# Performance work log

Hardware: AMD Instinct MI355X
Metric: run time of the kernel (lower is better)

## Reference

```python
import jax, jax.numpy as jnp
import numpy as np

B = 16       # number of point clouds
N_PER = 2048 # points per cloud
K = 16       # knn neighbors (loop=True -> self included as nearest)
NUM_CLASSES = 10


def _linear_params(key, fan_in, fan_out):
    # torch.nn.Linear default init: U(-1/sqrt(fan_in), 1/sqrt(fan_in))
    kw, kb = jax.random.split(key)
    s = 1.0 / np.sqrt(fan_in)
    W = jax.random.uniform(kw, (fan_in, fan_out), jnp.float32, -s, s)
    b = jax.random.uniform(kb, (fan_out,), jnp.float32, -s, s)
    return W, b


def setup_inputs() -> dict:
    key = jax.random.key(0)
    ks = jax.random.split(key, 7)
    pos = jax.random.normal(ks[0], (B * N_PER, 3), jnp.float32)
    batch = jnp.repeat(jnp.arange(B, dtype=jnp.int64), N_PER)  # sorted graph ids
    W1a, b1a = _linear_params(ks[1], 3 + 3, 32)   # conv1 mlp layer 1 (h=pos -> 3+3)
    W1b, b1b = _linear_params(ks[2], 32, 32)      # conv1 mlp layer 2
    W2a, b2a = _linear_params(ks[3], 32 + 3, 32)  # conv2 mlp layer 1
    W2b, b2b = _linear_params(ks[4], 32, 32)      # conv2 mlp layer 2
    Wc, bc = _linear_params(ks[5], 32, NUM_CLASSES)
    return dict(pos=pos, batch=batch,
                W1a=W1a, b1a=b1a, W1b=W1b, b1b=b1b,
                W2a=W2a, b2a=b2a, W2b=W2b, b2b=b2b,
                Wc=Wc, bc=bc)


def _knn_idx(p):
    # p: [n,3] -> [n,K] indices of K nearest points (self included, dist 0)
    d2 = jnp.sum((p[:, None, :] - p[None, :, :]) ** 2, axis=-1)  # [n,n]
    _, idx = jax.lax.top_k(-d2, K)
    return idx


def _pointnet_layer(h, p, idx, Wa, ba, Wb, bb):
    # single graph: h [n,C], p [n,3], idx [n,K]
    h_j = h[idx]                           # gather neighbor features [n,K,C]
    spatial = p[idx] - p[:, None, :]       # pos_j - pos_i [n,K,3]
    x = jnp.concatenate([h_j, spatial], axis=-1)
    x = jax.nn.relu(x @ Wa + ba) @ Wb + bb # per-edge MLP
    return jnp.max(x, axis=1)              # max aggregation over neighbors


def reference(pos, batch, W1a, b1a, W1b, b1b, W2a, b2a, W2b, b2b, Wc, bc):
    # batch is sorted with equal-sized graphs -> reshape to [B, n, 3]
    p = pos.reshape(B, N_PER, 3)
    idx = jax.vmap(_knn_idx)(p)  # [B, n, K] dynamic knn graph
    layer = jax.vmap(_pointnet_layer, in_axes=(0, 0, 0, None, None, None, None))
    h = jax.nn.relu(layer(p, p, idx, W1a, b1a, W1b, b1b))   # [B, n, 32]
    h = jax.nn.relu(layer(h, p, idx, W2a, b2a, W2b, b2b))   # [B, n, 32]
    g = jnp.max(h, axis=1)                                   # global_max_pool [B, 32]
    return g @ Wc + bc                                       # [B, num_classes]
```

## Files before the change

kernel.cpp:

```cpp
#include <hip/hip_runtime.h>
#include <hip/hip_bf16.h>
#include <cstdint>

#define NCLOUDS 16
#define N_PER   2048
#define KNN_K   16
#define CAP     48

typedef unsigned long long u64;
#define INFF __builtin_inff()

template <int J>
__device__ __forceinline__ int ixor(int x) {
    if constexpr (J == 1)
        return __builtin_amdgcn_update_dpp(0, x, 0xB1, 0xF, 0xF, true);
    else if constexpr (J == 2)
        return __builtin_amdgcn_update_dpp(0, x, 0x4E, 0xF, 0xF, true);
    else if constexpr (J <= 16)
        return __builtin_amdgcn_ds_swizzle(x, (J << 10) | 0x1F);
    else
        return __shfl_xor(x, 32);
}
template <int J> __device__ __forceinline__ float fxor(float x) {
    return __int_as_float(ixor<J>(__float_as_int(x)));
}
template <int J> __device__ __forceinline__ u64 uxor(u64 x) {
    const int lo = ixor<J>((int)(x & 0xffffffffULL));
    const int hi = ixor<J>((int)(x >> 32));
    return ((u64)(unsigned)hi << 32) | (unsigned)lo;
}

__device__ __forceinline__ float dpp_max16(float x) {
    x = fmaxf(x, __int_as_float(__builtin_amdgcn_update_dpp(0, __float_as_int(x), 0xB1, 0xF, 0xF, true)));
    x = fmaxf(x, __int_as_float(__builtin_amdgcn_update_dpp(0, __float_as_int(x), 0x4E, 0xF, 0xF, true)));
    x = fmaxf(x, __int_as_float(__builtin_amdgcn_update_dpp(0, __float_as_int(x), 0x141, 0xF, 0xF, true)));
    x = fmaxf(x, __int_as_float(__builtin_amdgcn_update_dpp(0, __float_as_int(x), 0x140, 0xF, 0xF, true)));
    return x;
}

__global__ __launch_bounds__(512) void knn_kernel(const float* __restrict__ pos,
                                                  int* __restrict__ knn_out,
                                                  const float* __restrict__ W1a,
                                                  const float* __restrict__ b1a,
                                                  float* __restrict__ w1,
                                                  float* __restrict__ v1)
{
    __shared__ float qshare[3][32];
    __shared__ float smA[4][2][8][16];
    __shared__ u64   buf[4][8][CAP];
    __shared__ int   cnt[4][8];

    const int cloud = blockIdx.x >> 6;
    const int qblk  = blockIdx.x & 63;
    const int tid   = threadIdx.x;
    const int wave  = tid >> 6;
    const int lane  = tid & 63;
    const int H     = wave & 1;
    const int pr    = wave >> 1;

    const int b0 = cloud * N_PER;

    if (tid < 32) {
        const float* qp = pos + (size_t)(b0 + qblk * 32 + tid) * 3;
        qshare[0][tid] = qp[0];
        qshare[1][tid] = qp[1];
        qshare[2][tid] = qp[2];
        ((int*)cnt)[tid] = 0;
    }

    float cx[16], cy[16], cz[16], sc[16];
#pragma unroll
    for (int jj = 0; jj < 16; ++jj) {
        const int c = H * 1024 + jj * 64 + lane;
        const float* p = pos + (size_t)(b0 + c) * 3;
        cx[jj] = p[0]; cy[jj] = p[1]; cz[jj] = p[2];
        sc[jj] = fmaf(cz[jj], cz[jj], fmaf(cy[jj], cy[jj], cx[jj] * cx[jj]));
    }
    __syncthreads();

#pragma unroll 1
    for (int t = 0; t < 4; ++t) {
        const int qg0 = pr * 8 + 2 * t, qg1 = qg0 + 1;
        const float Q0x = qshare[0][qg0], Q0y = qshare[1][qg0], Q0z = qshare[2][qg0];
        const float Q1x = qshare[0][qg1], Q1y = qshare[1][qg1], Q1z = qshare[2][qg1];
        const float A0x = -2.0f * Q0x, A0y = -2.0f * Q0y, A0z = -2.0f * Q0z;
        const float A1x = -2.0f * Q1x, A1y = -2.0f * Q1y, A1z = -2.0f * Q1z;
        float v0 = INFF, v1r = INFF;
#pragma unroll
        for (int jj = 0; jj < 16; ++jj) {
            float e0 = fmaf(cx[jj], A0x, sc[jj]);
            float e1 = fmaf(cx[jj], A1x, sc[jj]);
            e0 = fmaf(cy[jj], A0y, e0);  e1 = fmaf(cy[jj], A1y, e1);
            e0 = fmaf(cz[jj], A0z, e0);  e1 = fmaf(cz[jj], A1z, e1);
            v0 = fminf(v0, e0);          v1r = fminf(v1r, e1);
        }
#define FS(K, J) { const float o0 = fxor<J>(v0), o1 = fxor<J>(v1r);             \
                   const bool km = (((lane & J) == 0) == ((lane & K) == 0));    \
                   v0 = km ? fminf(v0, o0) : fmaxf(v0, o0);                     \
                   v1r = km ? fminf(v1r, o1) : fmaxf(v1r, o1); }
        FS(2,1)
        FS(4,2) FS(4,1)
        FS(8,4) FS(8,2) FS(8,1)
        FS(16,8) FS(16,4) FS(16,2) FS(16,1)
        FS(32,16) FS(32,8) FS(32,4) FS(32,2) FS(32,1)
        FS(64,32) FS(64,16) FS(64,8) FS(64,4) FS(64,2) FS(64,1)
#undef FS
        if (lane < 16) {
            smA[pr][H][2 * t][lane]     = v0;
            smA[pr][H][2 * t + 1][lane] = v1r;
        }
    }
    __syncthreads();

#pragma unroll 1
    for (int t = 0; t < 4; ++t) {
        const int q0 = 2 * t, q1 = q0 + 1;
        float a0 = -INFF, a1 = -INFF, b0v = -INFF, b1v = -INFF;
        if (lane > 0 && lane <= 16) {
            a0 = smA[pr][0][q0][lane - 1];
            a1 = smA[pr][0][q1][lane - 1];
        }
        if (lane < 16) {
            b0v = smA[pr][1][q0][15 - lane];
            b1v = smA[pr][1][q1][15 - lane];
        }
        float m0 = (lane <= 16) ? fmaxf(a0, b0v) : INFF;
        float m1 = (lane <= 16) ? fmaxf(a1, b1v) : INFF;
        m0 = fminf(m0, fxor<1>(m0));   m1 = fminf(m1, fxor<1>(m1));
        m0 = fminf(m0, fxor<2>(m0));   m1 = fminf(m1, fxor<2>(m1));
        m0 = fminf(m0, fxor<4>(m0));   m1 = fminf(m1, fxor<4>(m1));
        m0 = fminf(m0, fxor<8>(m0));   m1 = fminf(m1, fxor<8>(m1));
        m0 = fminf(m0, fxor<16>(m0));  m1 = fminf(m1, fxor<16>(m1));
        m0 = fminf(m0, fxor<32>(m0));  m1 = fminf(m1, fxor<32>(m1));

        const int qg0 = pr * 8 + q0, qg1 = pr * 8 + q1;
        const float Q0x = qshare[0][qg0], Q0y = qshare[1][qg0], Q0z = qshare[2][qg0];
        const float Q1x = qshare[0][qg1], Q1y = qshare[1][qg1], Q1z = qshare[2][qg1];
        const float qq0 = fmaf(Q0z, Q0z, fmaf(Q0y, Q0y, Q0x * Q0x));
        const float qq1 = fmaf(Q1z, Q1z, fmaf(Q1y, Q1y, Q1x * Q1x));
        const float T0 = (m0 + qq0) * (1.0f + 1e-5f) + 1e-4f;
        const float T1 = (m1 + qq1) * (1.0f + 1e-5f) + 1e-4f;

#pragma unroll
        for (int jj = 0; jj < 16; ++jj) {
            const int c = H * 1024 + jj * 64 + lane;
            const float dx0 = __fsub_rn(Q0x, cx[jj]);
            const float dy0 = __fsub_rn(Q0y, cy[jj]);
            const float dz0 = __fsub_rn(Q0z, cz[jj]);
            const float d20 = __fadd_rn(__fadd_rn(__fmul_rn(dx0, dx0), __fmul_rn(dy0, dy0)),
                                        __fmul_rn(dz0, dz0));
            if (d20 <= T0) {
                const int slot = atomicAdd(&cnt[pr][q0], 1);
                if (slot < CAP)
                    buf[pr][q0][slot] = ((u64)__float_as_uint(d20) << 32) | (unsigned)c;
            }
            const float dx1 = __fsub_rn(Q1x, cx[jj]);
            const float dy1 = __fsub_rn(Q1y, cy[jj]);
            const float dz1 = __fsub_rn(Q1z, cz[jj]);
            const float d21 = __fadd_rn(__fadd_rn(__fmul_rn(dx1, dx1), __fmul_rn(dy1, dy1)),
                                        __fmul_rn(dz1, dz1));
            if (d21 <= T1) {
                const int slot = atomicAdd(&cnt[pr][q1], 1);
                if (slot < CAP)
                    buf[pr][q1][slot] = ((u64)__float_as_uint(d21) << 32) | (unsigned)c;
            }
        }
    }
    __syncthreads();

#pragma unroll 1
    for (int s = 0; s < 2; ++s) {
        const int q0 = H * 4 + 2 * s, q1 = q0 + 1;
        const int n0 = min(cnt[pr][q0], CAP);
        const int n1 = min(cnt[pr][q1], CAP);
        u64 k0 = (lane < n0) ? buf[pr][q0][lane] : ~0ULL;
        u64 k1 = (lane < n1) ? buf[pr][q1][lane] : ~0ULL;
#define US(K, J) { const u64 o0 = uxor<J>(k0), o1 = uxor<J>(k1);                \
                   const bool km = (((lane & J) == 0) == ((lane & K) == 0));    \
                   const u64 l0 = k0 < o0 ? k0 : o0, h0 = k0 < o0 ? o0 : k0;    \
                   k0 = km ? l0 : h0;                                           \
                   const u64 l1 = k1 < o1 ? k1 : o1, h1 = k1 < o1 ? o1 : k1;    \
                   k1 = km ? l1 : h1; }
        US(2,1)
        US(4,2) US(4,1)
        US(8,4) US(8,2) US(8,1)
        US(16,8) US(16,4) US(16,2) US(16,1)
        US(32,16) US(32,8) US(32,4) US(32,2) US(32,1)
        US(64,32) US(64,16) US(64,8) US(64,4) US(64,2) US(64,1)
#undef US
        if (lane < KNN_K) {
            knn_out[((size_t)b0 + qblk * 32 + pr * 8 + q0) * KNN_K + lane] =
                b0 + (int)(unsigned)(k0 & 0xffffffffu);
            knn_out[((size_t)b0 + qblk * 32 + pr * 8 + q1) * KNN_K + lane] =
                b0 + (int)(unsigned)(k1 & 0xffffffffu);
        }
    }

    {
        const int pt = tid >> 4;
        const int kk = tid & 15;
        const int gp = b0 + qblk * 32 + pt;
        const float p0 = pos[3 * (size_t)gp + 0];
        const float p1 = pos[3 * (size_t)gp + 1];
        const float p2 = pos[3 * (size_t)gp + 2];
        float vA = 0.f, vB = 0.f;
        float wA = b1a[kk], wB = b1a[16 + kk];
#pragma unroll
        for (int d = 0; d < 3; ++d) {
            const float pd = d == 0 ? p0 : (d == 1 ? p1 : p2);
            wA = fmaf(pd, W1a[d * 32 + kk],        wA);
            wB = fmaf(pd, W1a[d * 32 + 16 + kk],   wB);
            vA = fmaf(pd, W1a[(3 + d) * 32 + kk],      vA);
            vB = fmaf(pd, W1a[(3 + d) * 32 + 16 + kk], vB);
        }
        w1[(size_t)gp * 32 + kk]      = wA + vA;
        w1[(size_t)gp * 32 + 16 + kk] = wB + vB;
        v1[(size_t)gp * 32 + kk]      = vA;
        v1[(size_t)gp * 32 + 16 + kk] = vB;
    }
}

template <bool FUSE_PRE2>
__global__ __launch_bounds__(256) void layer_kernel(
    const int*   __restrict__ knn,
    const float* __restrict__ Wb, const float* __restrict__ bb,
    const float* __restrict__ w,  const float* __restrict__ v,
    const float* __restrict__ pos,
    const float* __restrict__ Wna, const float* __restrict__ bna,
    float* __restrict__ outA, float* __restrict__ outB)
{
    __shared__ float h1s[16][32];

    const int gth = blockIdx.x * 256 + threadIdx.x;
    const int p = gth >> 4;
    const int k = gth & 15;
    const int j = knn[gth];

    const float4* w4 = (const float4*)w;
    const float4* v4 = (const float4*)v;

    float hid[32];
#pragma unroll
    for (int i = 0; i < 8; ++i) {
        const float4 a = w4[(size_t)j * 8 + i];
        const float4 b = v4[(size_t)p * 8 + i];
        hid[4 * i + 0] = fmaxf(a.x - b.x, 0.0f);
        hid[4 * i + 1] = fmaxf(a.y - b.y, 0.0f);
        hid[4 * i + 2] = fmaxf(a.z - b.z, 0.0f);
        hid[4 * i + 3] = fmaxf(a.w - b.w, 0.0f);
    }

    float o[32];
#pragma unroll
    for (int c2 = 0; c2 < 32; ++c2) o[c2] = bb[c2];
#pragma unroll
    for (int c = 0; c < 32; ++c) {
        const float hc = hid[c];
        const float* row = Wb + c * 32;
#pragma unroll
        for (int c2 = 0; c2 < 32; ++c2) o[c2] = fmaf(hc, row[c2], o[c2]);
    }

    float out0 = 0.0f, out1 = 0.0f;
#pragma unroll
    for (int c2 = 0; c2 < 32; ++c2) {
        const float s = dpp_max16(o[c2]);
        if ((c2 & 15) == k) { if (c2 < 16) out0 = s; else out1 = s; }
    }
    out0 = fmaxf(out0, 0.0f);
    out1 = fmaxf(out1, 0.0f);

    if constexpr (!FUSE_PRE2) {
        outA[(size_t)p * 32 + k]      = out0;
        outA[(size_t)p * 32 + 16 + k] = out1;
    } else {
        const int pl = threadIdx.x >> 4;
        h1s[pl][k]      = out0;
        h1s[pl][16 + k] = out1;
        __syncthreads();
        float accA = bna[k], accB = bna[16 + k];
#pragma unroll
        for (int c = 0; c < 32; ++c) {
            const float hc = h1s[pl][c];
            accA = fmaf(hc, Wna[c * 32 + k],      accA);
            accB = fmaf(hc, Wna[c * 32 + 16 + k], accB);
        }
        float vA = 0.f, vB = 0.f;
#pragma unroll
        for (int d = 0; d < 3; ++d) {
            const float pd = pos[3 * (size_t)p + d];
            vA = fmaf(pd, Wna[(32 + d) * 32 + k],      vA);
            vB = fmaf(pd, Wna[(32 + d) * 32 + 16 + k], vB);
        }
        outA[(size_t)p * 32 + k]      = accA + vA;
        outA[(size_t)p * 32 + 16 + k] = accB + vB;
        outB[(size_t)p * 32 + k]      = vA;
        outB[(size_t)p * 32 + 16 + k] = vB;
    }
}

__global__ __launch_bounds__(256) void pool_kernel(
    const float* __restrict__ h2, const float* __restrict__ Wc,
    const float* __restrict__ bc, float* __restrict__ out)
{
    __shared__ float red[8][32];
    __shared__ float sg[32];
    const int cloud = blockIdx.x;
    const int t = threadIdx.x;
    const int c = t & 31, row = t >> 5;
    float m = 0.0f;
    for (int p = row; p < N_PER; p += 8)
        m = fmaxf(m, h2[((size_t)cloud * N_PER + p) * 32 + c]);
    red[row][c] = m;
    __syncthreads();
    if (t < 32) {
        float gv = red[0][t];
#pragma unroll
        for (int r = 1; r < 8; ++r) gv = fmaxf(gv, red[r][t]);
        sg[t] = gv;
    }
    __syncthreads();
    if (t < 10) {
        float s = bc[t];
#pragma unroll
        for (int c0 = 0; c0 < 32; ++c0) s = fmaf(sg[c0], Wc[c0 * 10 + t], s);
        out[cloud * 10 + t] = s;
    }
}

extern "C" void kernel_launch(void* const* d_in, const int* in_sizes, int n_in,
                              void* d_out, int out_size, void* d_ws, size_t ws_size,
                              hipStream_t stream)
{
    const float* pos = (const float*)d_in[0];
    const float* W1a = (const float*)d_in[2];
    const float* b1a = (const float*)d_in[3];
    const float* W1b = (const float*)d_in[4];
    const float* b1b = (const float*)d_in[5];
    const float* W2a = (const float*)d_in[6];
    const float* b2a = (const float*)d_in[7];
    const float* W2b = (const float*)d_in[8];
    const float* b2b = (const float*)d_in[9];
    const float* Wc  = (const float*)d_in[10];
    const float* bc  = (const float*)d_in[11];

    int*   knn = (int*)d_ws;
    float* w1  = (float*)((char*)d_ws + (size_t)(2  << 20));
    float* v1  = (float*)((char*)d_ws + (size_t)(6  << 20));
    float* w2  = (float*)((char*)d_ws + (size_t)(10 << 20));
    float* v2  = (float*)((char*)d_ws + (size_t)(14 << 20));
    float* h2  = (float*)((char*)d_ws + (size_t)(18 << 20));
    float* out = (float*)d_out;

    const int npts = NCLOUDS * N_PER;

    knn_kernel<<<dim3(NCLOUDS * 64), dim3(512), 0, stream>>>(
        pos, knn, W1a, b1a, w1, v1);
    layer_kernel<true><<<dim3(npts * KNN_K / 256), dim3(256), 0, stream>>>(
        knn, W1b, b1b, w1, v1, pos, W2a, b2a, w2, v2);
    layer_kernel<false><<<dim3(npts * KNN_K / 256), dim3(256), 0, stream>>>(
        knn, W2b, b2b, w2, v2, pos, W2a, b2a, h2, nullptr);
    pool_kernel<<<dim3(NCLOUDS), dim3(256), 0, stream>>>(h2, Wc, bc, out);
}
```

Measured before the change: 151.1 us.

## Fuse global max-pool and classifier into layer-2 kernel; stage gathers in LDS

The separate pool kernel is removed. The second layer kernel now reduces its 16 points per block, does an atomicMax into a global buffer that the knn kernel zeroes, and the last block, found through an atomic counter, computes the classifier. Neighbor feature gathers are also staged into padded shared memory with cooperative float4 loads before the per-edge MLP. This saves one launch and the h2 write and read, at the cost of atomics, more LDS use (about 38KB per block, which may limit occupancy) and extra syncs.

```diff
diff --git a/kernel.cpp b/kernel.cpp
--- a/kernel.cpp
+++ b/kernel.cpp
@@ -43,7 +43,9 @@
                                                   const float* __restrict__ W1a,
                                                   const float* __restrict__ b1a,
                                                   float* __restrict__ w1,
-                                                  float* __restrict__ v1)
+                                                  float* __restrict__ v1,
+                                                  float* __restrict__ gbuf,
+                                                  int* __restrict__ counter)
 {
     __shared__ float qshare[3][32];
     __shared__ float smA[4][2][8][16];
@@ -59,6 +61,11 @@
     const int pr    = wave >> 1;
 
     const int b0 = cloud * N_PER;
+
+    if (blockIdx.x == 0) {
+        if (tid < NCLOUDS * 32) gbuf[tid] = 0.0f;
+        if (tid == 0) *counter = 0;
+    }
 
     if (tid < 32) {
         const float* qp = pos + (size_t)(b0 + qblk * 32 + tid) * 3;
@@ -220,30 +227,52 @@
     }
 }
 
-template <bool FUSE_PRE2>
+template <int MODE>
 __global__ __launch_bounds__(256) void layer_kernel(
     const int*   __restrict__ knn,
     const float* __restrict__ Wb, const float* __restrict__ bb,
     const float* __restrict__ w,  const float* __restrict__ v,
     const float* __restrict__ pos,
     const float* __restrict__ Wna, const float* __restrict__ bna,
-    float* __restrict__ outA, float* __restrict__ outB)
+    float* __restrict__ outA, float* __restrict__ outB,
+    const float* __restrict__ Wc, const float* __restrict__ bc,
+    float* __restrict__ gbuf, int* __restrict__ counter,
+    float* __restrict__ out)
 {
-    __shared__ float h1s[16][32];
-
-    const int gth = blockIdx.x * 256 + threadIdx.x;
-    const int p = gth >> 4;
-    const int k = gth & 15;
-    const int j = knn[gth];
-
-    const float4* w4 = (const float4*)w;
-    const float4* v4 = (const float4*)v;
+    __shared__ float wst[256 * 36];
+    __shared__ float vst[16 * 36];
+    __shared__ int   jl[256];
+    __shared__ int   lastFlag;
+
+    const int tid = threadIdx.x;
+    const int gth = blockIdx.x * 256 + tid;
+    const int P0  = blockIdx.x * 16;
+
+    jl[tid] = knn[gth];
+    __syncthreads();
+
+#pragma unroll
+    for (int s = 0; s < 8; ++s) {
+        const int r = s * 32 + (tid >> 3);
+        const int i = tid & 7;
+        const float4 t4 = *(const float4*)(w + (size_t)jl[r] * 32 + i * 4);
+        *(float4*)&wst[r * 36 + i * 4] = t4;
+    }
+    if (tid < 128) {
+        const int r = tid >> 3, i = tid & 7;
+        const float4 t4 = *(const float4*)(v + (size_t)(P0 + r) * 32 + i * 4);
+        *(float4*)&vst[r * 36 + i * 4] = t4;
+    }
+    __syncthreads();
+
+    const int k  = tid & 15;
+    const int pl = tid >> 4;
 
     float hid[32];
 #pragma unroll
     for (int i = 0; i < 8; ++i) {
-        const float4 a = w4[(size_t)j * 8 + i];
-        const float4 b = v4[(size_t)p * 8 + i];
+        const float4 a = *(const float4*)&wst[tid * 36 + i * 4];
+        const float4 b = *(const float4*)&vst[pl  * 36 + i * 4];
         hid[4 * i + 0] = fmaxf(a.x - b.x, 0.0f);
         hid[4 * i + 1] = fmaxf(a.y - b.y, 0.0f);
         hid[4 * i + 2] = fmaxf(a.z - b.z, 0.0f);
@@ -270,18 +299,18 @@
     out0 = fmaxf(out0, 0.0f);
     out1 = fmaxf(out1, 0.0f);
 
-    if constexpr (!FUSE_PRE2) {
-        outA[(size_t)p * 32 + k]      = out0;
-        outA[(size_t)p * 32 + 16 + k] = out1;
-    } else {
-        const int pl = threadIdx.x >> 4;
-        h1s[pl][k]      = out0;
-        h1s[pl][16 + k] = out1;
-        __syncthreads();
+    __syncthreads();
+    float* hs = wst;
+    hs[pl * 32 + k]      = out0;
+    hs[pl * 32 + 16 + k] = out1;
+    __syncthreads();
+
+    if constexpr (MODE == 1) {
+        const int p = gth >> 4;
         float accA = bna[k], accB = bna[16 + k];
 #pragma unroll
         for (int c = 0; c < 32; ++c) {
-            const float hc = h1s[pl][c];
+            const float hc = hs[pl * 32 + c];
             accA = fmaf(hc, Wna[c * 32 + k],      accA);
             accB = fmaf(hc, Wna[c * 32 + 16 + k], accB);
         }
@@ -296,35 +325,34 @@
         outA[(size_t)p * 32 + 16 + k] = accB + vB;
         outB[(size_t)p * 32 + k]      = vA;
         outB[(size_t)p * 32 + 16 + k] = vB;
-    }
-}
-
-__global__ __launch_bounds__(256) void pool_kernel(
-    const float* __restrict__ h2, const float* __restrict__ Wc,
-    const float* __restrict__ bc, float* __restrict__ out)
-{
-    __shared__ float red[8][32];
-    __shared__ float sg[32];
-    const int cloud = blockIdx.x;
-    const int t = threadIdx.x;
-    const int c = t & 31, row = t >> 5;
-    float m = 0.0f;
-    for (int p = row; p < N_PER; p += 8)
-        m = fmaxf(m, h2[((size_t)cloud * N_PER + p) * 32 + c]);
-    red[row][c] = m;
-    __syncthreads();
-    if (t < 32) {
-        float gv = red[0][t];
-#pragma unroll
-        for (int r = 1; r < 8; ++r) gv = fmaxf(gv, red[r][t]);
-        sg[t] = gv;
-    }
-    __syncthreads();
-    if (t < 10) {
-        float s = bc[t];
-#pragma unroll
-        for (int c0 = 0; c0 < 32; ++c0) s = fmaf(sg[c0], Wc[c0 * 10 + t], s);
-        out[cloud * 10 + t] = s;
+    } else {
+        if (tid < 32) {
+            float m = hs[tid];
+#pragma unroll
+            for (int p2 = 1; p2 < 16; ++p2) m = fmaxf(m, hs[p2 * 32 + tid]);
+            const int cloud = P0 >> 11;
+            atomicMax((int*)&gbuf[cloud * 32 + tid], __float_as_int(m));
+        }
+        __syncthreads();
+        if (tid == 0) {
+            __threadfence();
+            lastFlag = (atomicAdd(counter, 1) == (int)gridDim.x - 1);
+        }
+        __syncthreads();
+        if (lastFlag) {
+            float* gl = wst;
+            for (int t = tid; t < NCLOUDS * 32; t += 256)
+                gl[t] = __int_as_float(atomicMax((int*)&gbuf[t], 0));
+            __syncthreads();
+            if (tid < NCLOUDS * 10) {
+                const int cl = tid / 10, cls = tid - cl * 10;
+                float s2 = bc[cls];
+#pragma unroll
+                for (int c = 0; c < 32; ++c)
+                    s2 = fmaf(gl[cl * 32 + c], Wc[c * 10 + cls], s2);
+                out[tid] = s2;
+            }
+        }
     }
 }
 
@@ -344,21 +372,23 @@
     const float* Wc  = (const float*)d_in[10];
     const float* bc  = (const float*)d_in[11];
 
-    int*   knn = (int*)d_ws;
-    float* w1  = (float*)((char*)d_ws + (size_t)(2  << 20));
-    float* v1  = (float*)((char*)d_ws + (size_t)(6  << 20));
-    float* w2  = (float*)((char*)d_ws + (size_t)(10 << 20));
-    float* v2  = (float*)((char*)d_ws + (size_t)(14 << 20));
-    float* h2  = (float*)((char*)d_ws + (size_t)(18 << 20));
-    float* out = (float*)d_out;
+    int*   knn     = (int*)d_ws;
+    float* w1      = (float*)((char*)d_ws + (size_t)(2  << 20));
+    float* v1      = (float*)((char*)d_ws + (size_t)(6  << 20));
+    float* w2      = (float*)((char*)d_ws + (size_t)(10 << 20));
+    float* v2      = (float*)((char*)d_ws + (size_t)(14 << 20));
+    float* gbuf    = (float*)((char*)d_ws + (size_t)(18 << 20));
+    int*   counter = (int*)((char*)d_ws + (size_t)(18 << 20) + 4096);
+    float* out     = (float*)d_out;
 
     const int npts = NCLOUDS * N_PER;
 
     knn_kernel<<<dim3(NCLOUDS * 64), dim3(512), 0, stream>>>(
-        pos, knn, W1a, b1a, w1, v1);
-    layer_kernel<true><<<dim3(npts * KNN_K / 256), dim3(256), 0, stream>>>(
-        knn, W1b, b1b, w1, v1, pos, W2a, b2a, w2, v2);
-    layer_kernel<false><<<dim3(npts * KNN_K / 256), dim3(256), 0, stream>>>(
-        knn, W2b, b2b, w2, v2, pos, W2a, b2a, h2, nullptr);
-    pool_kernel<<<dim3(NCLOUDS), dim3(256), 0, stream>>>(h2, Wc, bc, out);
-}
+        pos, knn, W1a, b1a, w1, v1, gbuf, counter);
+    layer_kernel<1><<<dim3(npts * KNN_K / 256), dim3(256), 0, stream>>>(
+        knn, W1b, b1b, w1, v1, pos, W2a, b2a, w2, v2,
+        nullptr, nullptr, nullptr, nullptr, nullptr);
+    layer_kernel<2><<<dim3(npts * KNN_K / 256), dim3(256), 0, stream>>>(
+        knn, W2b, b2b, w2, v2, pos, nullptr, nullptr, nullptr, nullptr,
+        Wc, bc, gbuf, counter, out);
+}
```

After: 138.7 us. 1.09x faster.
